# Kernel optimization log

Hardware: AMD Instinct MI355X
Metric: run time of the kernel (lower is better)

## Reference

```python
import jax, jax.numpy as jnp
import numpy as np

ALPHA = 0.25
GAMMA = 2.0
VAR = jnp.array([0.1, 0.1, 0.2, 0.2], dtype=jnp.float32)  # bbox target normalization


def cal_iou(a, b):
    """Pairwise IoU between anchors a [A,4] and gt boxes b [M,4] (x1,y1,x2,y2)."""
    area_a = (a[:, 2] - a[:, 0]) * (a[:, 3] - a[:, 1])  # [A]
    area_b = (b[:, 2] - b[:, 0]) * (b[:, 3] - b[:, 1])  # [M]
    iw = jnp.clip(jnp.minimum(a[:, None, 2], b[None, :, 2]) - jnp.maximum(a[:, None, 0], b[None, :, 0]), 0.0)
    ih = jnp.clip(jnp.minimum(a[:, None, 3], b[None, :, 3]) - jnp.maximum(a[:, None, 1], b[None, :, 1]), 0.0)
    inter = iw * ih  # [A,M]
    union = jnp.clip(area_a[:, None] + area_b[None, :] - inter, 1e-8)
    return inter / union


def _per_image(pred_cls, pred_loc, anno, anchors):
    # pred_cls [A,K], pred_loc [A,4], anno [M,5], anchors [A,4]
    K = pred_cls.shape[1]
    labels = anno[:, 4]
    valid = labels != -1.0                      # [M] padding mask
    n_valid = valid.sum()

    pred_cls = jnp.clip(pred_cls, 1e-4, 1.0 - 1e-4)

    iou = cal_iou(anchors, anno[:, :4])         # [A,M]
    iou = jnp.where(valid[None, :], iou, -1.0)  # invalid gts never match
    iou_max = iou.max(axis=1)                   # [A]
    iou_arg = iou.argmax(axis=1)                # [A]
    gt = anno[iou_arg]                          # [A,5] matched gt per anchor

    pos = iou_max >= 0.5                        # [A]
    neg = iou_max < 0.4                         # [A]
    pos_num = pos.sum()

    lab = gt[:, 4].astype(jnp.int32)            # [A]
    onehot_pos = (jnp.arange(K)[None, :] == lab[:, None]).astype(pred_cls.dtype)
    # -1 = ignore, 0 = background, one-hot for positives
    onehot = jnp.where(pos[:, None], onehot_pos,
                       jnp.where(neg[:, None], 0.0, -1.0))

    alpha_t = jnp.where(onehot == 1.0, ALPHA, 1.0 - ALPHA)
    pt = jnp.where(onehot == 1.0, pred_cls, 1.0 - pred_cls)
    focal_w = alpha_t * (1.0 - pt) ** GAMMA
    bce = -(onehot * jnp.log(pred_cls) + (1.0 - onehot) * jnp.log(1.0 - pred_cls))
    cls = jnp.where(onehot == -1.0, 0.0, focal_w * bce)
    cls_loss = cls.sum() / jnp.maximum(pos_num.astype(pred_cls.dtype), 1.0)

    aw = anchors[:, 2] - anchors[:, 0]
    ah = anchors[:, 3] - anchors[:, 1]
    acx = anchors[:, 0] + 0.5 * aw
    acy = anchors[:, 1] + 0.5 * ah
    gw_raw = gt[:, 2] - gt[:, 0]
    gh_raw = gt[:, 3] - gt[:, 1]
    gcx = gt[:, 0] + 0.5 * gw_raw
    gcy = gt[:, 1] + 0.5 * gh_raw
    gw = jnp.maximum(gw_raw, 1.0)
    gh = jnp.maximum(gh_raw, 1.0)
    d = jnp.stack([(gcx - acx) / aw, (gcy - acy) / ah,
                   jnp.log(gw / aw), jnp.log(gh / ah)], axis=1) / VAR  # [A,4]
    diff = jnp.abs(d - pred_loc)
    sl1 = jnp.where(diff <= 1.0 / 9.0, 0.5 * 9.0 * diff ** 2, diff - 0.5 / 9.0)
    denom = jnp.maximum(pos_num.astype(pred_cls.dtype) * 4.0, 1.0)
    loc_loss = (sl1 * pos[:, None].astype(pred_cls.dtype)).sum() / denom
    loc_loss = jnp.where(pos_num > 0, loc_loss, 0.0)

    has_anno = n_valid > 0
    return jnp.where(has_anno, cls_loss, 0.0), jnp.where(has_anno, loc_loss, 0.0)


def setup_inputs() -> dict:
    key = jax.random.key(0)
    k1, k2, k3, k4, k5, k6 = jax.random.split(key, 6)
    B, A, K, M = 8, 100000, 80, 32
    classification = jax.random.uniform(k1, (B, A, K), dtype=jnp.float32)
    localization = jax.random.normal(k2, (B, A, 4), dtype=jnp.float32)
    # anchors: x1,y1 in [0,800), w,h in [16,272)
    axy = jax.random.uniform(k3, (A, 2), dtype=jnp.float32) * 800.0
    awh = jax.random.uniform(k4, (A, 2), dtype=jnp.float32) * 256.0 + 16.0
    anchors = jnp.concatenate([axy, axy + awh], axis=1)
    gxy = jax.random.uniform(k5, (B, M, 2), dtype=jnp.float32) * 800.0
    gwh = jax.random.uniform(jax.random.fold_in(k5, 1), (B, M, 2), dtype=jnp.float32) * 256.0 + 16.0
    glab = jax.random.randint(k6, (B, M, 1), 0, K).astype(jnp.float32)
    annotations = jnp.concatenate([gxy, gxy + gwh, glab], axis=2)  # [B,M,5]
    return {"classification": classification, "localization": localization,
            "anchors": anchors, "annotations": annotations}


def reference(classification, localization, anchors, annotations):
    cls_l, loc_l = jax.vmap(_per_image, in_axes=(0, 0, 0, None))(
        classification, localization, annotations, anchors)
    return (cls_l.mean(keepdims=True), loc_l.mean(keepdims=True))
```

## Files before the change

kernel.cpp:

```cpp
#include <hip/hip_runtime.h>

#define BLK 256
#define ANCH 256

constexpr float LN2 = 0.6931471805599453f;

__device__ __forceinline__ float bg4(const float4 v) {
    const float pv[4] = { v.x, v.y, v.z, v.w };
    float acc = 0.0f;
#pragma unroll
    for (int i = 0; i < 4; ++i) {
        const float p = fminf(fmaxf(pv[i], 0.0001f), 1.0f - 0.0001f);
        acc = fmaf(p * p, __log2f(1.0f - p), acc);
    }
    return acc;
}

__device__ __forceinline__ void quad(const float4 v, const int st, const int c0,
                                     float& cls_part) {
    const float s = bg4(v);
    cls_part = fmaf(s, (st == 255) ? 0.0f : -0.75f * LN2, cls_part);
    const unsigned d = (unsigned)(st - c0);
    if (d < 4u) {
        float p = v.x;
        p = (d == 1) ? v.y : p;
        p = (d == 2) ? v.z : p;
        p = (d == 3) ? v.w : p;
        p = fminf(fmaxf(p, 0.0001f), 1.0f - 0.0001f);
        const float bg = p * p * __log2f(1.0f - p);
        const float q  = 1.0f - p;
        const float fg = q * q * __log2f(p);
        cls_part += -LN2 * (0.25f * fg - 0.75f * bg);
    }
}

template <int KQ_C, int M_C>
__global__ __launch_bounds__(BLK) void focal_main(
    const float* __restrict__ cls,
    const float* __restrict__ loc,
    const float* __restrict__ anchors,
    const float* __restrict__ anno,
    int A, int kq_dyn, int m_dyn, int B, int NBX,
    float* __restrict__ part)
{
    const int KQ = KQ_C ? KQ_C : kq_dyn;
    const int M  = M_C  ? M_C  : m_dyn;
    const int b  = blockIdx.y;
    const int bx = blockIdx.x;
    const int a0 = bx * ANCH;
    const int t  = threadIdx.x;
    const int nA = min(ANCH, A - a0);

    __shared__ float4 s_box[64];
    __shared__ float  s_lab[64];
    __shared__ int    s_status[ANCH];
    __shared__ float  s_redc[BLK / 64];
    __shared__ float  s_redl[BLK / 64];
    __shared__ float  s_redp[BLK / 64];

    const float4* __restrict__ cls4 =
        reinterpret_cast<const float4*>(cls) + ((size_t)b * A + a0) * KQ;
    const bool full = (KQ_C == 20) && (nA == ANCH);

#define LOADB(R, BK)                                                        \
    do {                                                                    \
        _Pragma("unroll") for (int u_ = 0; u_ < 4; ++u_)                    \
            R[u_] = cls4[t + ((BK) * 4 + u_) * BLK];                        \
    } while (0)

#define EVALB(R, BK)                                                        \
    do {                                                                    \
        _Pragma("unroll") for (int u_ = 0; u_ < 4; ++u_) {                  \
            const int idx_ = t + ((BK) * 4 + u_) * BLK;                     \
            const int al_  = idx_ / 20;                                     \
            const int c0_  = (idx_ - al_ * 20) * 4;                         \
            quad(R[u_], s_status[al_], c0_, cls_part);                      \
        }                                                                   \
    } while (0)

    float4 va[4], vb[4];
    if (full) { LOADB(va, 0); LOADB(vb, 1); }

    if (t < M) {
        const float* ap = anno + ((size_t)b * M + t) * 5;
        s_box[t] = make_float4(ap[0], ap[1], ap[2], ap[3]);
        s_lab[t] = ap[4];
    }
    __syncthreads();

    float loc_part = 0.0f;
    float pos_part = 0.0f;

    if (t < nA) {
        const int a = a0 + t;
        const float4 anc = reinterpret_cast<const float4*>(anchors)[a];
        const float ax1 = anc.x, ay1 = anc.y, ax2 = anc.z, ay2 = anc.w;
        const float area_a = (ax2 - ax1) * (ay2 - ay1);

        float best = -1e30f;
        int arg = 0;
#pragma unroll
        for (int m = 0; m < M; ++m) {
            const float4 bb = s_box[m];
            const float lb  = s_lab[m];
            float iou;
            if (lb != -1.0f) {
                const float area_b = (bb.z - bb.x) * (bb.w - bb.y);
                const float iw = fmaxf(fminf(ax2, bb.z) - fmaxf(ax1, bb.x), 0.0f);
                const float ih = fmaxf(fminf(ay2, bb.w) - fmaxf(ay1, bb.y), 0.0f);
                const float inter = iw * ih;
                const float uni = fmaxf(area_a + area_b - inter, 1e-8f);
                iou = inter / uni;
            } else {
                iou = -1.0f;
            }
            if (iou > best) { best = iou; arg = m; }
        }

        const bool pos = best >= 0.5f;
        const bool neg = best < 0.4f;
        s_status[t] = pos ? (int)s_lab[arg] : (neg ? 254 : 255);

        if (pos) {
            pos_part = 1.0f;
            const float4 g = s_box[arg];
            const float aw = ax2 - ax1, ah = ay2 - ay1;
            const float acx = ax1 + 0.5f * aw, acy = ay1 + 0.5f * ah;
            const float gwr = g.z - g.x, ghr = g.w - g.y;
            const float gcx = g.x + 0.5f * gwr, gcy = g.y + 0.5f * ghr;
            const float gw = fmaxf(gwr, 1.0f), gh = fmaxf(ghr, 1.0f);
            const float d0 = ((gcx - acx) / aw) / 0.1f;
            const float d1 = ((gcy - acy) / ah) / 0.1f;
            const float d2 = __logf(gw / aw) / 0.2f;
            const float d3 = __logf(gh / ah) / 0.2f;
            const float4 pl = reinterpret_cast<const float4*>(loc)[(size_t)b * A + a];
            const float df[4] = { fabsf(d0 - pl.x), fabsf(d1 - pl.y),
                                  fabsf(d2 - pl.z), fabsf(d3 - pl.w) };
#pragma unroll
            for (int i = 0; i < 4; ++i) {
                const float d = df[i];
                loc_part += (d <= (1.0f / 9.0f)) ? (0.5f * 9.0f) * d * d
                                                 : d - (0.5f / 9.0f);
            }
        }
    } else if (t < ANCH) {
        s_status[t] = 255;
    }
    __syncthreads();

    float cls_part = 0.0f;
    if (full) {
        EVALB(va, 0); LOADB(va, 2);
        EVALB(vb, 1); LOADB(vb, 3);
        EVALB(va, 2); LOADB(va, 4);
        EVALB(vb, 3);
        EVALB(va, 4);
    } else {
        const int total = nA * KQ;
        for (int idx = t; idx < total; idx += BLK) {
            const float4 v = cls4[idx];
            const int al = idx / KQ;
            const int c0 = (idx - al * KQ) * 4;
            quad(v, s_status[al], c0, cls_part);
        }
    }

#pragma unroll
    for (int off = 32; off > 0; off >>= 1) {
        cls_part += __shfl_down(cls_part, off);
        loc_part += __shfl_down(loc_part, off);
        pos_part += __shfl_down(pos_part, off);
    }
    const int wid = t >> 6;
    if ((t & 63) == 0) {
        s_redc[wid] = cls_part;
        s_redl[wid] = loc_part;
        s_redp[wid] = pos_part;
    }
    __syncthreads();
    if (t == 0) {
        float c = 0.0f, l = 0.0f, p = 0.0f;
#pragma unroll
        for (int w = 0; w < BLK / 64; ++w) { c += s_redc[w]; l += s_redl[w]; p += s_redp[w]; }
        part[(size_t)b * NBX + bx]           = c;
        part[(size_t)(B + b) * NBX + bx]     = l;
        part[(size_t)(2 * B + b) * NBX + bx] = p;
    }
#undef LOADB
#undef EVALB
}

__global__ void focal_final(const float* __restrict__ anno, int B, int M, int NBX,
                            const float* __restrict__ part,
                            float* __restrict__ out)
{
    __shared__ float s_c[32], s_l[32];
    const int t = threadIdx.x;
    const int lane = t & 31;
    const int ngrp = blockDim.x >> 5;
    if (t < 32) { s_c[t] = 0.0f; s_l[t] = 0.0f; }
    __syncthreads();

    for (int img = t >> 5; img < B; img += ngrp) {
        float c = 0.0f, l = 0.0f, p = 0.0f, nv = 0.0f;
        const float* pc = part + (size_t)img * NBX;
        const float* pl = part + (size_t)(B + img) * NBX;
        const float* pp = part + (size_t)(2 * B + img) * NBX;
        for (int e = lane; e < NBX; e += 32) { c += pc[e]; l += pl[e]; p += pp[e]; }
        for (int m = lane; m < M; m += 32)
            nv += (anno[((size_t)img * M + m) * 5 + 4] != -1.0f) ? 1.0f : 0.0f;
#pragma unroll
        for (int off = 16; off > 0; off >>= 1) {
            c  += __shfl_down(c,  off, 32);
            l  += __shfl_down(l,  off, 32);
            p  += __shfl_down(p,  off, 32);
            nv += __shfl_down(nv, off, 32);
        }
        if (lane == 0) {
            float cls_l = c / fmaxf(p, 1.0f);
            float loc_l = (p > 0.0f) ? l / fmaxf(4.0f * p, 1.0f) : 0.0f;
            if (nv == 0.0f) { cls_l = 0.0f; loc_l = 0.0f; }
            s_c[img] = cls_l;
            s_l[img] = loc_l;
        }
    }
    __syncthreads();
    if (t == 0) {
        float cs = 0.0f, ls = 0.0f;
        for (int i = 0; i < B; ++i) { cs += s_c[i]; ls += s_l[i]; }
        out[0] = cs / (float)B;
        out[1] = ls / (float)B;
    }
}

extern "C" void kernel_launch(void* const* d_in, const int* in_sizes, int n_in,
                              void* d_out, int out_size, void* d_ws, size_t ws_size,
                              hipStream_t stream) {
    const float* cls     = (const float*)d_in[0];
    const float* loc     = (const float*)d_in[1];
    const float* anchors = (const float*)d_in[2];
    const float* anno    = (const float*)d_in[3];

    const int A  = in_sizes[2] / 4;
    const long long BA = (long long)in_sizes[1] / 4;
    const int B  = (int)(BA / A);
    const int K  = (int)((long long)in_sizes[0] / BA);
    const int M  = in_sizes[3] / (B * 5);
    const int KQ = K >> 2;
    const int NBX = (A + ANCH - 1) / ANCH;

    float* part = (float*)d_ws;

    dim3 grid(NBX, B);
    if (KQ == 20 && M == 32) {
        focal_main<20, 32><<<grid, BLK, 0, stream>>>(cls, loc, anchors, anno,
                                                     A, KQ, M, B, NBX, part);
    } else {
        focal_main<0, 0><<<grid, BLK, 0, stream>>>(cls, loc, anchors, anno,
                                                   A, KQ, M, B, NBX, part);
    }
    focal_final<<<1, 256, 0, stream>>>(anno, B, M, NBX, part, (float*)d_out);
}
```

Baseline: 58.68 us.

## Double anchors per block, remove IoU division, deepen classification prefetch pipeline

Each block now handles 512 anchors with 256 threads, so every thread matches two anchors. The classification stream is prefetched three batches deep instead of two. IoU argmax now compares inter/union pairs by cross-multiplication, which removes the per-gt division, and invalid gts get a NaN area that makes the comparison fail. The aim is to cut division cost, halve the block count and per-block overhead, and keep more loads in flight, at the cost of extra registers and lower occupancy. The NaN trick and the changed tie handling could slightly alter argmax semantics.

```diff
diff --git a/kernel.cpp b/kernel.cpp
--- a/kernel.cpp
+++ b/kernel.cpp
@@ -1,7 +1,7 @@
 #include <hip/hip_runtime.h>
 
 #define BLK 256
-#define ANCH 256
+#define ANCH 512
 
 constexpr float LN2 = 0.6931471805599453f;
 
@@ -52,6 +52,7 @@
     const int nA = min(ANCH, A - a0);
 
     __shared__ float4 s_box[64];
+    __shared__ float  s_area[64];
     __shared__ float  s_lab[64];
     __shared__ int    s_status[ANCH];
     __shared__ float  s_redc[BLK / 64];
@@ -61,6 +62,16 @@
     const float4* __restrict__ cls4 =
         reinterpret_cast<const float4*>(cls) + ((size_t)b * A + a0) * KQ;
     const bool full = (KQ_C == 20) && (nA == ANCH);
+
+    if (t < M) {
+        const float* ap = anno + ((size_t)b * M + t) * 5;
+        const float x1 = ap[0], y1 = ap[1], x2 = ap[2], y2 = ap[3], lb = ap[4];
+        s_box[t]  = make_float4(x1, y1, x2, y2);
+        s_area[t] = (lb != -1.0f) ? (x2 - x1) * (y2 - y1)
+                                  : __int_as_float(0x7fc00000);
+        s_lab[t]  = lb;
+    }
+    __syncthreads();
 
 #define LOADB(R, BK)                                                        \
     do {                                                                    \
@@ -78,83 +89,82 @@
         }                                                                   \
     } while (0)
 
-    float4 va[4], vb[4];
-    if (full) { LOADB(va, 0); LOADB(vb, 1); }
-
-    if (t < M) {
-        const float* ap = anno + ((size_t)b * M + t) * 5;
-        s_box[t] = make_float4(ap[0], ap[1], ap[2], ap[3]);
-        s_lab[t] = ap[4];
-    }
-    __syncthreads();
+    float4 va[4], vb[4], vc[4];
+    if (full) { LOADB(va, 0); LOADB(vb, 1); LOADB(vc, 2); }
 
     float loc_part = 0.0f;
     float pos_part = 0.0f;
 
-    if (t < nA) {
-        const int a = a0 + t;
-        const float4 anc = reinterpret_cast<const float4*>(anchors)[a];
-        const float ax1 = anc.x, ay1 = anc.y, ax2 = anc.z, ay2 = anc.w;
-        const float area_a = (ax2 - ax1) * (ay2 - ay1);
-
-        float best = -1e30f;
-        int arg = 0;
-#pragma unroll
-        for (int m = 0; m < M; ++m) {
-            const float4 bb = s_box[m];
-            const float lb  = s_lab[m];
-            float iou;
-            if (lb != -1.0f) {
-                const float area_b = (bb.z - bb.x) * (bb.w - bb.y);
+#pragma unroll
+    for (int s = 0; s < 2; ++s) {
+        const int al = t + s * BLK;
+        int st = 255;
+        if (al < nA) {
+            const int a = a0 + al;
+            const float4 anc = reinterpret_cast<const float4*>(anchors)[a];
+            const float ax1 = anc.x, ay1 = anc.y, ax2 = anc.z, ay2 = anc.w;
+            const float area_a = (ax2 - ax1) * (ay2 - ay1);
+
+            float bi = -2.0f, bu = 1.0f;
+            int arg = 0;
+#pragma unroll
+            for (int m = 0; m < M; ++m) {
+                const float4 bb = s_box[m];
+                const float ab  = s_area[m];
                 const float iw = fmaxf(fminf(ax2, bb.z) - fmaxf(ax1, bb.x), 0.0f);
                 const float ih = fmaxf(fminf(ay2, bb.w) - fmaxf(ay1, bb.y), 0.0f);
                 const float inter = iw * ih;
-                const float uni = fmaxf(area_a + area_b - inter, 1e-8f);
-                iou = inter / uni;
-            } else {
-                iou = -1.0f;
+                const float uni = fmaxf(area_a + ab - inter, 1e-8f);
+                const bool better = inter * bu > bi * uni;
+                bi  = better ? inter : bi;
+                bu  = better ? uni   : bu;
+                arg = better ? m     : arg;
             }
-            if (iou > best) { best = iou; arg = m; }
-        }
-
-        const bool pos = best >= 0.5f;
-        const bool neg = best < 0.4f;
-        s_status[t] = pos ? (int)s_lab[arg] : (neg ? 254 : 255);
-
-        if (pos) {
-            pos_part = 1.0f;
-            const float4 g = s_box[arg];
-            const float aw = ax2 - ax1, ah = ay2 - ay1;
-            const float acx = ax1 + 0.5f * aw, acy = ay1 + 0.5f * ah;
-            const float gwr = g.z - g.x, ghr = g.w - g.y;
-            const float gcx = g.x + 0.5f * gwr, gcy = g.y + 0.5f * ghr;
-            const float gw = fmaxf(gwr, 1.0f), gh = fmaxf(ghr, 1.0f);
-            const float d0 = ((gcx - acx) / aw) / 0.1f;
-            const float d1 = ((gcy - acy) / ah) / 0.1f;
-            const float d2 = __logf(gw / aw) / 0.2f;
-            const float d3 = __logf(gh / ah) / 0.2f;
-            const float4 pl = reinterpret_cast<const float4*>(loc)[(size_t)b * A + a];
-            const float df[4] = { fabsf(d0 - pl.x), fabsf(d1 - pl.y),
-                                  fabsf(d2 - pl.z), fabsf(d3 - pl.w) };
-#pragma unroll
-            for (int i = 0; i < 4; ++i) {
-                const float d = df[i];
-                loc_part += (d <= (1.0f / 9.0f)) ? (0.5f * 9.0f) * d * d
-                                                 : d - (0.5f / 9.0f);
+
+            const bool pos = bi >= 0.5f * bu;
+            const bool neg = bi <  0.4f * bu;
+            st = pos ? (int)s_lab[arg] : (neg ? 254 : 255);
+
+            if (pos) {
+                pos_part += 1.0f;
+                const float4 g = s_box[arg];
+                const float aw = ax2 - ax1, ah = ay2 - ay1;
+                const float acx = ax1 + 0.5f * aw, acy = ay1 + 0.5f * ah;
+                const float gwr = g.z - g.x, ghr = g.w - g.y;
+                const float gcx = g.x + 0.5f * gwr, gcy = g.y + 0.5f * ghr;
+                const float gw = fmaxf(gwr, 1.0f), gh = fmaxf(ghr, 1.0f);
+                const float d0 = ((gcx - acx) / aw) / 0.1f;
+                const float d1 = ((gcy - acy) / ah) / 0.1f;
+                const float d2 = __logf(gw / aw) / 0.2f;
+                const float d3 = __logf(gh / ah) / 0.2f;
+                const float4 pl =
+                    reinterpret_cast<const float4*>(loc)[(size_t)b * A + a];
+                const float df[4] = { fabsf(d0 - pl.x), fabsf(d1 - pl.y),
+                                      fabsf(d2 - pl.z), fabsf(d3 - pl.w) };
+#pragma unroll
+                for (int i = 0; i < 4; ++i) {
+                    const float d = df[i];
+                    loc_part += (d <= (1.0f / 9.0f)) ? (0.5f * 9.0f) * d * d
+                                                     : d - (0.5f / 9.0f);
+                }
             }
         }
-    } else if (t < ANCH) {
-        s_status[t] = 255;
+        s_status[al] = st;
     }
     __syncthreads();
 
     float cls_part = 0.0f;
     if (full) {
-        EVALB(va, 0); LOADB(va, 2);
-        EVALB(vb, 1); LOADB(vb, 3);
-        EVALB(va, 2); LOADB(va, 4);
-        EVALB(vb, 3);
-        EVALB(va, 4);
+        EVALB(va, 0); LOADB(va, 3);
+        EVALB(vb, 1); LOADB(vb, 4);
+        EVALB(vc, 2); LOADB(vc, 5);
+        EVALB(va, 3); LOADB(va, 6);
+        EVALB(vb, 4); LOADB(vb, 7);
+        EVALB(vc, 5); LOADB(vc, 8);
+        EVALB(va, 6); LOADB(va, 9);
+        EVALB(vb, 7);
+        EVALB(vc, 8);
+        EVALB(va, 9);
     } else {
         const int total = nA * KQ;
         for (int idx = t; idx < total; idx += BLK) {
```

After: 64.09 us. +9.2%, slower.

## Fuse final reduction via last-block atomic counter and drop IoU division

Applied to the files above, without the earlier changes.

The separate final reduction kernel is removed. Each block now bumps a global atomic counter after writing its partial sums, and the last block to finish performs the cross-image reduction, which saves a kernel launch at the cost of a memset and a threadfence/atomic per block. The IoU argmax loop replaces the per-gt division with cross-multiplied comparisons of intersection and union, and invalid boxes are handled with a precomputed NaN area. The annotation load and its sync also move ahead of the classification prefetch.

```diff
diff --git a/kernel.cpp b/kernel.cpp
--- a/kernel.cpp
+++ b/kernel.cpp
@@ -41,7 +41,9 @@
     const float* __restrict__ anchors,
     const float* __restrict__ anno,
     int A, int kq_dyn, int m_dyn, int B, int NBX,
-    float* __restrict__ part)
+    float* __restrict__ part,
+    unsigned int* __restrict__ counter,
+    float* __restrict__ out)
 {
     const int KQ = KQ_C ? KQ_C : kq_dyn;
     const int M  = M_C  ? M_C  : m_dyn;
@@ -52,15 +54,27 @@
     const int nA = min(ANCH, A - a0);
 
     __shared__ float4 s_box[64];
+    __shared__ float  s_area[64];
     __shared__ float  s_lab[64];
     __shared__ int    s_status[ANCH];
     __shared__ float  s_redc[BLK / 64];
     __shared__ float  s_redl[BLK / 64];
     __shared__ float  s_redp[BLK / 64];
+    __shared__ int    s_islast;
 
     const float4* __restrict__ cls4 =
         reinterpret_cast<const float4*>(cls) + ((size_t)b * A + a0) * KQ;
     const bool full = (KQ_C == 20) && (nA == ANCH);
+
+    if (t < M) {
+        const float* ap = anno + ((size_t)b * M + t) * 5;
+        const float x1 = ap[0], y1 = ap[1], x2 = ap[2], y2 = ap[3], lb = ap[4];
+        s_box[t]  = make_float4(x1, y1, x2, y2);
+        s_area[t] = (lb != -1.0f) ? (x2 - x1) * (y2 - y1)
+                                  : __int_as_float(0x7fc00000);
+        s_lab[t]  = lb;
+    }
+    __syncthreads();
 
 #define LOADB(R, BK)                                                        \
     do {                                                                    \
@@ -81,13 +95,6 @@
     float4 va[4], vb[4];
     if (full) { LOADB(va, 0); LOADB(vb, 1); }
 
-    if (t < M) {
-        const float* ap = anno + ((size_t)b * M + t) * 5;
-        s_box[t] = make_float4(ap[0], ap[1], ap[2], ap[3]);
-        s_lab[t] = ap[4];
-    }
-    __syncthreads();
-
     float loc_part = 0.0f;
     float pos_part = 0.0f;
 
@@ -97,28 +104,24 @@
         const float ax1 = anc.x, ay1 = anc.y, ax2 = anc.z, ay2 = anc.w;
         const float area_a = (ax2 - ax1) * (ay2 - ay1);
 
-        float best = -1e30f;
+        float bi = -2.0f, bu = 1.0f;
         int arg = 0;
 #pragma unroll
         for (int m = 0; m < M; ++m) {
             const float4 bb = s_box[m];
-            const float lb  = s_lab[m];
-            float iou;
-            if (lb != -1.0f) {
-                const float area_b = (bb.z - bb.x) * (bb.w - bb.y);
-                const float iw = fmaxf(fminf(ax2, bb.z) - fmaxf(ax1, bb.x), 0.0f);
-                const float ih = fmaxf(fminf(ay2, bb.w) - fmaxf(ay1, bb.y), 0.0f);
-                const float inter = iw * ih;
-                const float uni = fmaxf(area_a + area_b - inter, 1e-8f);
-                iou = inter / uni;
-            } else {
-                iou = -1.0f;
-            }
-            if (iou > best) { best = iou; arg = m; }
-        }
-
-        const bool pos = best >= 0.5f;
-        const bool neg = best < 0.4f;
+            const float ab  = s_area[m];
+            const float iw = fmaxf(fminf(ax2, bb.z) - fmaxf(ax1, bb.x), 0.0f);
+            const float ih = fmaxf(fminf(ay2, bb.w) - fmaxf(ay1, bb.y), 0.0f);
+            const float inter = iw * ih;
+            const float uni = fmaxf(area_a + ab - inter, 1e-8f);
+            const bool better = inter * bu > bi * uni;
+            bi  = better ? inter : bi;
+            bu  = better ? uni   : bu;
+            arg = better ? m     : arg;
+        }
+
+        const bool pos = bi >= 0.5f * bu;
+        const bool neg = bi <  0.4f * bu;
         s_status[t] = pos ? (int)s_lab[arg] : (neg ? 254 : 255);
 
         if (pos) {
@@ -178,6 +181,7 @@
         s_redp[wid] = pos_part;
     }
     __syncthreads();
+    const unsigned int nblk = (unsigned int)(B * NBX);
     if (t == 0) {
         float c = 0.0f, l = 0.0f, p = 0.0f;
 #pragma unroll
@@ -185,52 +189,52 @@
         part[(size_t)b * NBX + bx]           = c;
         part[(size_t)(B + b) * NBX + bx]     = l;
         part[(size_t)(2 * B + b) * NBX + bx] = p;
+        __threadfence();
+        const unsigned int old = atomicAdd(counter, 1u);
+        s_islast = (old == nblk - 1u) ? 1 : 0;
+    }
+    __syncthreads();
+
+    if (s_islast) {
+        __threadfence();
+        __shared__ float f_c[64], f_l[64];
+        const int lane = t & 31;
+        const int ngrp = BLK >> 5;
+        if (t < 64) { f_c[t] = 0.0f; f_l[t] = 0.0f; }
+        __syncthreads();
+        for (int img = t >> 5; img < B; img += ngrp) {
+            float c = 0.0f, l = 0.0f, p = 0.0f, nv = 0.0f;
+            const float* pc = part + (size_t)img * NBX;
+            const float* pl = part + (size_t)(B + img) * NBX;
+            const float* pp = part + (size_t)(2 * B + img) * NBX;
+            for (int e = lane; e < NBX; e += 32) { c += pc[e]; l += pl[e]; p += pp[e]; }
+            for (int m = lane; m < M; m += 32)
+                nv += (anno[((size_t)img * M + m) * 5 + 4] != -1.0f) ? 1.0f : 0.0f;
+#pragma unroll
+            for (int off = 16; off > 0; off >>= 1) {
+                c  += __shfl_down(c,  off, 32);
+                l  += __shfl_down(l,  off, 32);
+                p  += __shfl_down(p,  off, 32);
+                nv += __shfl_down(nv, off, 32);
+            }
+            if (lane == 0) {
+                float cls_l = c / fmaxf(p, 1.0f);
+                float loc_l = (p > 0.0f) ? l / fmaxf(4.0f * p, 1.0f) : 0.0f;
+                if (nv == 0.0f) { cls_l = 0.0f; loc_l = 0.0f; }
+                f_c[img] = cls_l;
+                f_l[img] = loc_l;
+            }
+        }
+        __syncthreads();
+        if (t == 0) {
+            float cs = 0.0f, ls = 0.0f;
+            for (int i = 0; i < B; ++i) { cs += f_c[i]; ls += f_l[i]; }
+            out[0] = cs / (float)B;
+            out[1] = ls / (float)B;
+        }
     }
 #undef LOADB
 #undef EVALB
-}
-
-__global__ void focal_final(const float* __restrict__ anno, int B, int M, int NBX,
-                            const float* __restrict__ part,
-                            float* __restrict__ out)
-{
-    __shared__ float s_c[32], s_l[32];
-    const int t = threadIdx.x;
-    const int lane = t & 31;
-    const int ngrp = blockDim.x >> 5;
-    if (t < 32) { s_c[t] = 0.0f; s_l[t] = 0.0f; }
-    __syncthreads();
-
-    for (int img = t >> 5; img < B; img += ngrp) {
-        float c = 0.0f, l = 0.0f, p = 0.0f, nv = 0.0f;
-        const float* pc = part + (size_t)img * NBX;
-        const float* pl = part + (size_t)(B + img) * NBX;
-        const float* pp = part + (size_t)(2 * B + img) * NBX;
-        for (int e = lane; e < NBX; e += 32) { c += pc[e]; l += pl[e]; p += pp[e]; }
-        for (int m = lane; m < M; m += 32)
-            nv += (anno[((size_t)img * M + m) * 5 + 4] != -1.0f) ? 1.0f : 0.0f;
-#pragma unroll
-        for (int off = 16; off > 0; off >>= 1) {
-            c  += __shfl_down(c,  off, 32);
-            l  += __shfl_down(l,  off, 32);
-            p  += __shfl_down(p,  off, 32);
-            nv += __shfl_down(nv, off, 32);
-        }
-        if (lane == 0) {
-            float cls_l = c / fmaxf(p, 1.0f);
-            float loc_l = (p > 0.0f) ? l / fmaxf(4.0f * p, 1.0f) : 0.0f;
-            if (nv == 0.0f) { cls_l = 0.0f; loc_l = 0.0f; }
-            s_c[img] = cls_l;
-            s_l[img] = loc_l;
-        }
-    }
-    __syncthreads();
-    if (t == 0) {
-        float cs = 0.0f, ls = 0.0f;
-        for (int i = 0; i < B; ++i) { cs += s_c[i]; ls += s_l[i]; }
-        out[0] = cs / (float)B;
-        out[1] = ls / (float)B;
-    }
 }
 
 extern "C" void kernel_launch(void* const* d_in, const int* in_sizes, int n_in,
@@ -250,14 +254,18 @@
     const int NBX = (A + ANCH - 1) / ANCH;
 
     float* part = (float*)d_ws;
+    unsigned int* counter = (unsigned int*)(part + (size_t)3 * B * NBX);
+
+    hipMemsetAsync(counter, 0, sizeof(unsigned int), stream);
 
     dim3 grid(NBX, B);
     if (KQ == 20 && M == 32) {
         focal_main<20, 32><<<grid, BLK, 0, stream>>>(cls, loc, anchors, anno,
-                                                     A, KQ, M, B, NBX, part);
+                                                     A, KQ, M, B, NBX, part,
+                                                     counter, (float*)d_out);
     } else {
         focal_main<0, 0><<<grid, BLK, 0, stream>>>(cls, loc, anchors, anno,
-                                                   A, KQ, M, B, NBX, part);
-    }
-    focal_final<<<1, 256, 0, stream>>>(anno, B, M, NBX, part, (float*)d_out);
-}
+                                                   A, KQ, M, B, NBX, part,
+                                                   counter, (float*)d_out);
+    }
+}
```

After: 172.6 us. 194% more time.
